# Optimization experiments

Hardware: AMD Instinct MI355X
Metric: run time of the kernel (lower is better)

## Reference

```python
import jax, jax.numpy as jnp
import numpy as np

B, C, H, W = 8, 256, 64, 64


def setup_inputs() -> dict:
    key = jax.random.key(0)
    ks = jax.random.split(key, 9)
    s = 1.0 / np.sqrt(C)  # conv2d default init scale
    return {
        "foreground": jax.random.normal(ks[0], (B, C, H, W), jnp.float32),
        "background": jax.random.normal(ks[1], (B, C, H, W), jnp.float32),
        "mask": jax.random.uniform(ks[2], (B, C, H, W), jnp.float32),
        "Wq": jax.random.normal(ks[3], (C, C), jnp.float32) * s,
        "bq": jnp.zeros((C,), jnp.float32),
        "Wk": jax.random.normal(ks[4], (C, C), jnp.float32) * s,
        "bk": jnp.zeros((C,), jnp.float32),
        "Wv": jax.random.normal(ks[5], (C, C), jnp.float32) * s,
        "bv": jnp.zeros((C,), jnp.float32),
        "gamma": jnp.ones((1,), jnp.float32),
    }


def _conv1x1(x, Wt, b):
    # 1x1 conv == per-pixel channel matmul; x: [B,C,H,W], Wt: [Cout,Cin]
    return jnp.einsum('bchw,oc->bohw', x, Wt) + b[None, :, None, None]


def reference(foreground, background, mask, Wq, bq, Wk, bk, Wv, bv, gamma):
    b, c, h, w = foreground.shape
    hw = h * w
    # mask is already at feature resolution (interpolate would be identity)
    q = _conv1x1(foreground, Wq, bq).reshape(b, c, hw)   # [B,C,HW]
    k = _conv1x1(background, Wk, bk).reshape(b, c, hw)   # [B,C,HW]
    # bmm(q, k^T): channel-channel correlation [B,C,C]
    corr = jnp.einsum('bci,bdi->bcd', q, k)
    m_r = mask.reshape(b, c, hw)                          # [B,C,HW]
    # bmm(corr, m_r): mask-modulated scores [B,C,HW]
    scores = jnp.einsum('bcd,bdi->bci', corr, m_r)
    energy = jax.nn.softmax(scores, axis=-1)
    v = _conv1x1(foreground, Wv, bv).reshape(b, c, hw)
    attended = (energy * v).reshape(b, c, h, w)
    out = foreground * mask + gamma[0] * (1.0 - mask) * attended
    return out
```

## Files before the change

### kernel.cpp

```cpp
#include <hip/hip_runtime.h>
#include <math.h>

#define B_    8
#define C_    256
#define HW_   4096
#define CHW_  ((long)C_ * HW_)

#define BKT   32
#define LDH   40
#define KS    16
#define KCH   (HW_ / KS)

typedef __attribute__((ext_vector_type(8))) short bf16x8;
typedef __attribute__((ext_vector_type(4))) float f32x4;
#define MFMA_BF16(a, b, c) __builtin_amdgcn_mfma_f32_16x16x32_bf16((a), (b), (c), 0, 0, 0)

__device__ __forceinline__ void cvt_hl4(const float4 f, uint* h, uint* l) {
    uint u0 = __float_as_uint(f.x), u1 = __float_as_uint(f.y),
         u2 = __float_as_uint(f.z), u3 = __float_as_uint(f.w);
    uint h0 = (u0 + 0x8000u) & 0xFFFF0000u, h1 = (u1 + 0x8000u) & 0xFFFF0000u,
         h2 = (u2 + 0x8000u) & 0xFFFF0000u, h3 = (u3 + 0x8000u) & 0xFFFF0000u;
    h[0] = (h0 >> 16) | h1;
    h[1] = (h2 >> 16) | h3;
    float l0 = f.x - __uint_as_float(h0), l1 = f.y - __uint_as_float(h1),
          l2 = f.z - __uint_as_float(h2), l3 = f.w - __uint_as_float(h3);
    uint a0 = __float_as_uint(l0) & 0xFFFF0000u, a1 = __float_as_uint(l1) & 0xFFFF0000u,
         a2 = __float_as_uint(l2) & 0xFFFF0000u, a3 = __float_as_uint(l3) & 0xFFFF0000u;
    l[0] = (a0 >> 16) | a1;
    l[1] = (a2 >> 16) | a3;
}
__device__ __forceinline__ void cvt_h4(const float4 f, uint* h) {
    uint u0 = __float_as_uint(f.x), u1 = __float_as_uint(f.y),
         u2 = __float_as_uint(f.z), u3 = __float_as_uint(f.w);
    uint h0 = (u0 + 0x8000u) & 0xFFFF0000u, h1 = (u1 + 0x8000u) & 0xFFFF0000u,
         h2 = (u2 + 0x8000u) & 0xFFFF0000u, h3 = (u3 + 0x8000u) & 0xFFFF0000u;
    h[0] = (h0 >> 16) | h1;
    h[1] = (h2 >> 16) | h3;
}

__global__ __launch_bounds__(256) void prep_hl(
    const float* __restrict__ fg, const float* __restrict__ bg,
    ushort* __restrict__ fgh, ushort* __restrict__ fgl,
    ushort* __restrict__ bgh, ushort* __restrict__ bgl,
    float* __restrict__ fsum, float* __restrict__ gsum)
{
    const int row = blockIdx.x;
    const int t   = threadIdx.x;
    const long base = (long)row * HW_;

    float sf = 0.0f, sg = 0.0f;
    #pragma unroll
    for (int j = 0; j < 4; ++j) {
        const int idx = (j * 256 + t) * 4;
        float4 a = *reinterpret_cast<const float4*>(&fg[base + idx]);
        float4 c = *reinterpret_cast<const float4*>(&bg[base + idx]);
        uint h[2], l[2];
        cvt_hl4(a, h, l);
        *reinterpret_cast<uint2*>(&fgh[base + idx]) = make_uint2(h[0], h[1]);
        *reinterpret_cast<uint2*>(&fgl[base + idx]) = make_uint2(l[0], l[1]);
        cvt_hl4(c, h, l);
        *reinterpret_cast<uint2*>(&bgh[base + idx]) = make_uint2(h[0], h[1]);
        *reinterpret_cast<uint2*>(&bgl[base + idx]) = make_uint2(l[0], l[1]);
        sf += a.x + a.y + a.z + a.w;
        sg += c.x + c.y + c.z + c.w;
    }
    #pragma unroll
    for (int o = 32; o > 0; o >>= 1) { sf += __shfl_xor(sf, o); sg += __shfl_xor(sg, o); }
    __shared__ float red[8];
    const int wid = t >> 6;
    if ((t & 63) == 0) { red[wid] = sf; red[4 + wid] = sg; }
    __syncthreads();
    if (t == 0) {
        fsum[row] = red[0] + red[1] + red[2] + red[3];
        gsum[row] = red[4] + red[5] + red[6] + red[7];
    }
}

__global__ __launch_bounds__(256) void conv_w(
    const float* __restrict__ Wv, ushort* __restrict__ Wvh)
{
    const int i = (blockIdx.x * 256 + threadIdx.x) * 4;
    float4 v = *reinterpret_cast<const float4*>(&Wv[i]);
    uint h[2];
    cvt_h4(v, h);
    *reinterpret_cast<uint2*>(&Wvh[i]) = make_uint2(h[0], h[1]);
}

__global__ __launch_bounds__(256) void conv_transpose(
    const float* __restrict__ mask, const float* __restrict__ fg,
    ushort* __restrict__ mTh, ushort* __restrict__ mTl, ushort* __restrict__ fTh)
{
    __shared__ float tile[64][65];
    const int zi = blockIdx.z;
    const bool domask = zi < B_;
    const int b = domask ? zi : zi - B_;
    const float* src = (domask ? mask : fg) + (long)b * CHW_;
    const int e0 = blockIdx.y * 64, i0 = blockIdx.x * 64;

    const int t  = threadIdx.x;
    const int tr = t >> 4, tc = (t & 15) * 4;

    #pragma unroll
    for (int j = 0; j < 4; ++j) {
        const int e = tr + j * 16;
        float4 v = *reinterpret_cast<const float4*>(&src[(long)(e0 + e) * HW_ + i0 + tc]);
        tile[e][tc + 0] = v.x; tile[e][tc + 1] = v.y;
        tile[e][tc + 2] = v.z; tile[e][tc + 3] = v.w;
    }
    __syncthreads();

    #pragma unroll
    for (int j = 0; j < 4; ++j) {
        const int i = tr + j * 16;
        float4 v = make_float4(tile[tc + 0][i], tile[tc + 1][i], tile[tc + 2][i], tile[tc + 3][i]);
        const long o = (long)b * CHW_ + (long)(i0 + i) * C_ + e0 + tc;
        if (domask) {
            uint h[2], l[2];
            cvt_hl4(v, h, l);
            *reinterpret_cast<uint2*>(&mTh[o]) = make_uint2(h[0], h[1]);
            *reinterpret_cast<uint2*>(&mTl[o]) = make_uint2(l[0], l[1]);
        } else {
            uint h[2];
            cvt_h4(v, h);
            *reinterpret_cast<uint2*>(&fTh[o]) = make_uint2(h[0], h[1]);
        }
    }
}

__global__ __launch_bounds__(256, 3) void gemm_nt_mfma(
    const ushort* __restrict__ Fh, const ushort* __restrict__ Fl,
    const ushort* __restrict__ Gh, const ushort* __restrict__ Gl,
    float* __restrict__ part)
{
    __shared__ ushort Ah[128 * LDH], Al[128 * LDH], Bh[128 * LDH], Bl[128 * LDH];

    const int z  = blockIdx.z;
    const int b  = z >> 4;
    const int ks = z & (KS - 1);
    const int c0 = blockIdx.y * 128;
    const int d0 = blockIdx.x * 128;
    const long boff = (long)b * CHW_ + (long)ks * KCH;

    const int t    = threadIdx.x;
    const int srow = t >> 1;
    const int sk   = (t & 1) * 16;
    const int lane = t & 63, w = t >> 6;
    const int col  = lane & 15, quad = lane >> 4;
    const int wm   = (w >> 1) * 64, wn = (w & 1) * 64;

    f32x4 acc[4][4] = {};

    for (int kt = 0; kt < KCH; kt += BKT) {
        const long ga = boff + (long)(c0 + srow) * HW_ + kt + sk;
        const long gb = boff + (long)(d0 + srow) * HW_ + kt + sk;
        uint4 ah0 = *reinterpret_cast<const uint4*>(&Fh[ga]);
        uint4 ah1 = *reinterpret_cast<const uint4*>(&Fh[ga + 8]);
        uint4 al0 = *reinterpret_cast<const uint4*>(&Fl[ga]);
        uint4 al1 = *reinterpret_cast<const uint4*>(&Fl[ga + 8]);
        uint4 bh0 = *reinterpret_cast<const uint4*>(&Gh[gb]);
        uint4 bh1 = *reinterpret_cast<const uint4*>(&Gh[gb + 8]);
        uint4 bl0 = *reinterpret_cast<const uint4*>(&Gl[gb]);
        uint4 bl1 = *reinterpret_cast<const uint4*>(&Gl[gb + 8]);
        *reinterpret_cast<uint4*>(&Ah[srow * LDH + sk])     = ah0;
        *reinterpret_cast<uint4*>(&Ah[srow * LDH + sk + 8]) = ah1;
        *reinterpret_cast<uint4*>(&Al[srow * LDH + sk])     = al0;
        *reinterpret_cast<uint4*>(&Al[srow * LDH + sk + 8]) = al1;
        *reinterpret_cast<uint4*>(&Bh[srow * LDH + sk])     = bh0;
        *reinterpret_cast<uint4*>(&Bh[srow * LDH + sk + 8]) = bh1;
        *reinterpret_cast<uint4*>(&Bl[srow * LDH + sk])     = bl0;
        *reinterpret_cast<uint4*>(&Bl[srow * LDH + sk + 8]) = bl1;
        __syncthreads();

        bf16x8 bfh[4], bfl[4];
        #pragma unroll
        for (int tj = 0; tj < 4; ++tj) {
            const int r = (wn + tj * 16 + col) * LDH + quad * 8;
            bfh[tj] = *reinterpret_cast<const bf16x8*>(&Bh[r]);
            bfl[tj] = *reinterpret_cast<const bf16x8*>(&Bl[r]);
        }
        #pragma unroll
        for (int ti = 0; ti < 4; ++ti) {
            const int r = (wm + ti * 16 + col) * LDH + quad * 8;
            bf16x8 afh = *reinterpret_cast<const bf16x8*>(&Ah[r]);
            bf16x8 afl = *reinterpret_cast<const bf16x8*>(&Al[r]);
            #pragma unroll
            for (int tj = 0; tj < 4; ++tj) {
                acc[ti][tj] = MFMA_BF16(afh, bfh[tj], acc[ti][tj]);
                acc[ti][tj] = MFMA_BF16(afh, bfl[tj], acc[ti][tj]);
                acc[ti][tj] = MFMA_BF16(afl, bfh[tj], acc[ti][tj]);
            }
        }
        __syncthreads();
    }

    float* P = part + (long)z * C_ * C_;
    #pragma unroll
    for (int ti = 0; ti < 4; ++ti) {
        const int m = c0 + wm + ti * 16 + quad * 4;
        #pragma unroll
        for (int tj = 0; tj < 4; ++tj) {
            const int n = d0 + wn + tj * 16 + col;
            #pragma unroll
            for (int r = 0; r < 4; ++r)
                P[(long)(m + r) * C_ + n] = acc[ti][tj][r];
        }
    }
}

__global__ __launch_bounds__(256, 3) void gemm_scores_mfma(
    const ushort* __restrict__ corrh, const ushort* __restrict__ corrl,
    const ushort* __restrict__ mTh,   const ushort* __restrict__ mTl,
    float* __restrict__ S)
{
    __shared__ ushort Ah[128 * LDH], Al[128 * LDH], Bh[128 * LDH], Bl[128 * LDH];

    const int b  = blockIdx.z;
    const int m0 = blockIdx.y * 128;
    const int n0 = blockIdx.x * 128;
    const ushort* Ahb = corrh + (long)b * C_ * C_;
    const ushort* Alb = corrl + (long)b * C_ * C_;
    const ushort* Bhb = mTh + (long)b * CHW_;
    const ushort* Blb = mTl + (long)b * CHW_;

    const int t    = threadIdx.x;
    const int srow = t >> 1;
    const int sk   = (t & 1) * 16;
    const int lane = t & 63, w = t >> 6;
    const int col  = lane & 15, quad = lane >> 4;
    const int wm   = (w >> 1) * 64, wn = (w & 1) * 64;

    f32x4 acc[4][4] = {};

    for (int kt = 0; kt < C_; kt += BKT) {
        const long ga = (long)(m0 + srow) * C_ + kt + sk;
        const long gb = (long)(n0 + srow) * C_ + kt + sk;
        uint4 ah0 = *reinterpret_cast<const uint4*>(&Ahb[ga]);
        uint4 ah1 = *reinterpret_cast<const uint4*>(&Ahb[ga + 8]);
        uint4 al0 = *reinterpret_cast<const uint4*>(&Alb[ga]);
        uint4 al1 = *reinterpret_cast<const uint4*>(&Alb[ga + 8]);
        uint4 bh0 = *reinterpret_cast<const uint4*>(&Bhb[gb]);
        uint4 bh1 = *reinterpret_cast<const uint4*>(&Bhb[gb + 8]);
        uint4 bl0 = *reinterpret_cast<const uint4*>(&Blb[gb]);
        uint4 bl1 = *reinterpret_cast<const uint4*>(&Blb[gb + 8]);
        *reinterpret_cast<uint4*>(&Ah[srow * LDH + sk])     = ah0;
        *reinterpret_cast<uint4*>(&Ah[srow * LDH + sk + 8]) = ah1;
        *reinterpret_cast<uint4*>(&Al[srow * LDH + sk])     = al0;
        *reinterpret_cast<uint4*>(&Al[srow * LDH + sk + 8]) = al1;
        *reinterpret_cast<uint4*>(&Bh[srow * LDH + sk])     = bh0;
        *reinterpret_cast<uint4*>(&Bh[srow * LDH + sk + 8]) = bh1;
        *reinterpret_cast<uint4*>(&Bl[srow * LDH + sk])     = bl0;
        *reinterpret_cast<uint4*>(&Bl[srow * LDH + sk + 8]) = bl1;
        __syncthreads();

        bf16x8 bfh[4], bfl[4];
        #pragma unroll
        for (int tj = 0; tj < 4; ++tj) {
            const int r = (wn + tj * 16 + col) * LDH + quad * 8;
            bfh[tj] = *reinterpret_cast<const bf16x8*>(&Bh[r]);
            bfl[tj] = *reinterpret_cast<const bf16x8*>(&Bl[r]);
        }
        #pragma unroll
        for (int ti = 0; ti < 4; ++ti) {
            const int r = (wm + ti * 16 + col) * LDH + quad * 8;
            bf16x8 afh = *reinterpret_cast<const bf16x8*>(&Ah[r]);
            bf16x8 afl = *reinterpret_cast<const bf16x8*>(&Al[r]);
            #pragma unroll
            for (int tj = 0; tj < 4; ++tj) {
                acc[ti][tj] = MFMA_BF16(afh, bfh[tj], acc[ti][tj]);
                acc[ti][tj] = MFMA_BF16(afh, bfl[tj], acc[ti][tj]);
                acc[ti][tj] = MFMA_BF16(afl, bfh[tj], acc[ti][tj]);
            }
        }
        __syncthreads();
    }

    float* Sb = S + (long)b * CHW_;
    #pragma unroll
    for (int ti = 0; ti < 4; ++ti) {
        const int m = m0 + wm + ti * 16 + quad * 4;
        #pragma unroll
        for (int tj = 0; tj < 4; ++tj) {
            const int n = n0 + wn + tj * 16 + col;
            #pragma unroll
            for (int r = 0; r < 4; ++r)
                Sb[(long)(m + r) * HW_ + n] = acc[ti][tj][r];
        }
    }
}

__global__ __launch_bounds__(256, 3) void gemm_v_final_mfma(
    const ushort* __restrict__ Wvh, const ushort* __restrict__ fTh,
    const float* __restrict__ bv, const float* __restrict__ fg,
    const float* __restrict__ mask, const float* __restrict__ S,
    const float* __restrict__ stats, const float* __restrict__ gamma,
    float* __restrict__ out)
{
    __shared__ ushort Ahh[128 * LDH], Bhh[128 * LDH];

    const int b  = blockIdx.z;
    const int m0 = blockIdx.y * 128;
    const int n0 = blockIdx.x * 128;
    const ushort* Bb = fTh + (long)b * CHW_;

    const int t    = threadIdx.x;
    const int srow = t >> 1;
    const int sk   = (t & 1) * 16;
    const int lane = t & 63, w = t >> 6;
    const int col  = lane & 15, quad = lane >> 4;
    const int wm   = (w >> 1) * 64, wn = (w & 1) * 64;

    f32x4 acc[4][4] = {};

    for (int kt = 0; kt < C_; kt += BKT) {
        const long ga = (long)(m0 + srow) * C_ + kt + sk;
        const long gb = (long)(n0 + srow) * C_ + kt + sk;
        uint4 a0 = *reinterpret_cast<const uint4*>(&Wvh[ga]);
        uint4 a1 = *reinterpret_cast<const uint4*>(&Wvh[ga + 8]);
        uint4 b0 = *reinterpret_cast<const uint4*>(&Bb[gb]);
        uint4 b1 = *reinterpret_cast<const uint4*>(&Bb[gb + 8]);
        *reinterpret_cast<uint4*>(&Ahh[srow * LDH + sk])     = a0;
        *reinterpret_cast<uint4*>(&Ahh[srow * LDH + sk + 8]) = a1;
        *reinterpret_cast<uint4*>(&Bhh[srow * LDH + sk])     = b0;
        *reinterpret_cast<uint4*>(&Bhh[srow * LDH + sk + 8]) = b1;
        __syncthreads();

        bf16x8 bfh[4];
        #pragma unroll
        for (int tj = 0; tj < 4; ++tj)
            bfh[tj] = *reinterpret_cast<const bf16x8*>(&Bhh[(wn + tj * 16 + col) * LDH + quad * 8]);
        #pragma unroll
        for (int ti = 0; ti < 4; ++ti) {
            bf16x8 afh = *reinterpret_cast<const bf16x8*>(&Ahh[(wm + ti * 16 + col) * LDH + quad * 8]);
            #pragma unroll
            for (int tj = 0; tj < 4; ++tj)
                acc[ti][tj] = MFMA_BF16(afh, bfh[tj], acc[ti][tj]);
        }
        __syncthreads();
    }

    const float g = gamma[0];
    #pragma unroll
    for (int ti = 0; ti < 4; ++ti) {
        const int m = m0 + wm + ti * 16 + quad * 4;
        #pragma unroll
        for (int r = 0; r < 4; ++r) {
            const int row  = b * C_ + m + r;
            const float mx  = stats[row];
            const float inv = 1.0f / stats[B_ * C_ + row];
            const float bvm = bv[m + r];
            #pragma unroll
            for (int tj = 0; tj < 4; ++tj) {
                const int n = n0 + wn + tj * 16 + col;
                const long e = (long)b * CHW_ + (long)(m + r) * HW_ + n;
                const float f  = fg[e];
                const float mk = mask[e];
                const float sv = S[e];
                const float vv = acc[ti][tj][r] + bvm;
                out[e] = f * mk + g * (1.0f - mk) * (__expf(sv - mx) * inv) * vv;
            }
        }
    }
}

__global__ __launch_bounds__(256) void reduce_part(
    const float* __restrict__ part, float* __restrict__ S1)
{
    const long idx = (long)blockIdx.x * 256 + threadIdx.x;
    const int  b   = (int)(idx >> 16);
    const long e   = idx & 65535;
    const float* p = part + ((long)b * KS) * 65536 + e;
    float s = 0.0f;
    #pragma unroll
    for (int ks = 0; ks < KS; ++ks) s += p[(long)ks * 65536];
    S1[idx] = s;
}

__global__ __launch_bounds__(256) void uvw_kernel(
    const float* __restrict__ Wq, const float* __restrict__ Wk,
    const float* __restrict__ bk,
    const float* __restrict__ fsum, const float* __restrict__ gsum,
    float* __restrict__ u, float* __restrict__ wh)
{
    const int g = blockIdx.x * 256 + threadIdx.x;
    if (g < 2048) {
        const int b = g >> 8, c = g & 255;
        const float* w = Wq + (long)c * C_;
        const float* s = fsum + b * C_;
        float acc = 0.0f;
        for (int e = 0; e < C_; ++e) acc = fmaf(w[e], s[e], acc);
        u[g] = acc;
    } else {
        const int g2 = g - 2048;
        const int b = g2 >> 8, d = g2 & 255;
        const float* w = Wk + (long)d * C_;
        const float* s = gsum + b * C_;
        float acc = 0.0f;
        for (int f = 0; f < C_; ++f) acc = fmaf(w[f], s[f], acc);
        wh[g2] = acc + (float)HW_ * bk[d];
    }
}

#define BK64 16
#define LDT64 68
__global__ __launch_bounds__(256) void gemm_nt64(
    const float* __restrict__ S1, const float* __restrict__ Wk,
    float* __restrict__ T)
{
    __shared__ float As[BK64][LDT64];
    __shared__ float Bs[BK64][LDT64];
    const int r0 = blockIdx.y * 64;
    const int d0 = blockIdx.x * 64;
    const int t   = threadIdx.x;
    const int tx  = t & 15, ty = t >> 4;
    const int tx4 = tx * 4, ty4 = ty * 4;
    const int am  = t >> 2, ak4 = (t & 3) * 4;

    float acc[4][4] = {};
    for (int k0 = 0; k0 < C_; k0 += BK64) {
        float4 av = *reinterpret_cast<const float4*>(&S1[(long)(r0 + am) * C_ + k0 + ak4]);
        float4 bw = *reinterpret_cast<const float4*>(&Wk[(long)(d0 + am) * C_ + k0 + ak4]);
        As[ak4+0][am]=av.x; As[ak4+1][am]=av.y; As[ak4+2][am]=av.z; As[ak4+3][am]=av.w;
        Bs[ak4+0][am]=bw.x; Bs[ak4+1][am]=bw.y; Bs[ak4+2][am]=bw.z; Bs[ak4+3][am]=bw.w;
        __syncthreads();
        #pragma unroll
        for (int kk = 0; kk < BK64; ++kk) {
            float4 a = *reinterpret_cast<const float4*>(&As[kk][ty4]);
            float4 x = *reinterpret_cast<const float4*>(&Bs[kk][tx4]);
            const float ar[4] = {a.x,a.y,a.z,a.w};
            const float xr[4] = {x.x,x.y,x.z,x.w};
            #pragma unroll
            for (int r = 0; r < 4; ++r)
                #pragma unroll
                for (int s = 0; s < 4; ++s)
                    acc[r][s] = fmaf(ar[r], xr[s], acc[r][s]);
        }
        __syncthreads();
    }
    #pragma unroll
    for (int r = 0; r < 4; ++r) {
        float4 o; o.x=acc[r][0]; o.y=acc[r][1]; o.z=acc[r][2]; o.w=acc[r][3];
        *reinterpret_cast<float4*>(&T[(long)(r0 + ty4 + r) * C_ + d0 + tx4]) = o;
    }
}

__global__ __launch_bounds__(256) void gemm_nn64_rank1(
    const float* __restrict__ Wq, const float* __restrict__ T,
    const float* __restrict__ u,  const float* __restrict__ bk,
    const float* __restrict__ bq, const float* __restrict__ wh,
    ushort* __restrict__ corrh, ushort* __restrict__ corrl)
{
    __shared__ float As[BK64][LDT64];
    __shared__ float Bs[BK64][LDT64];
    const int b  = blockIdx.z;
    const int m0 = blockIdx.y * 64;
    const int n0 = blockIdx.x * 64;
    const float* Tb = T + (long)b * C_ * C_;

    const int t   = threadIdx.x;
    const int tx  = t & 15, ty = t >> 4;
    const int tx4 = tx * 4, ty4 = ty * 4;
    const int am  = t >> 2, ak4 = (t & 3) * 4;
    const int xk  = ty,     xn4 = tx4;

    float acc[4][4] = {};
    for (int k0 = 0; k0 < C_; k0 += BK64) {
        float4 av = *reinterpret_cast<const float4*>(&Wq[(long)(m0 + am) * C_ + k0 + ak4]);
        float4 xv = *reinterpret_cast<const float4*>(&Tb[(long)(k0 + xk) * C_ + n0 + xn4]);
        As[ak4+0][am]=av.x; As[ak4+1][am]=av.y; As[ak4+2][am]=av.z; As[ak4+3][am]=av.w;
        *reinterpret_cast<float4*>(&Bs[xk][xn4]) = xv;
        __syncthreads();
        #pragma unroll
        for (int kk = 0; kk < BK64; ++kk) {
            float4 a = *reinterpret_cast<const float4*>(&As[kk][ty4]);
            float4 x = *reinterpret_cast<const float4*>(&Bs[kk][tx4]);
            const float ar[4] = {a.x,a.y,a.z,a.w};
            const float xr[4] = {x.x,x.y,x.z,x.w};
            #pragma unroll
            for (int r = 0; r < 4; ++r)
                #pragma unroll
                for (int s = 0; s < 4; ++s)
                    acc[r][s] = fmaf(ar[r], xr[s], acc[r][s]);
        }
        __syncthreads();
    }

    float4 bkv = *reinterpret_cast<const float4*>(&bk[n0 + tx4]);
    float4 whv = *reinterpret_cast<const float4*>(&wh[b * C_ + n0 + tx4]);
    #pragma unroll
    for (int r = 0; r < 4; ++r) {
        const int m = m0 + ty4 + r;
        const float um = u[b * C_ + m];
        const float bm = bq[m];
        float4 o;
        o.x = acc[r][0] + um*bkv.x + bm*whv.x;
        o.y = acc[r][1] + um*bkv.y + bm*whv.y;
        o.z = acc[r][2] + um*bkv.z + bm*whv.z;
        o.w = acc[r][3] + um*bkv.w + bm*whv.w;
        uint h[2], l[2];
        cvt_hl4(o, h, l);
        const long e = (long)b * C_ * C_ + (long)m * C_ + n0 + tx4;
        *reinterpret_cast<uint2*>(&corrh[e]) = make_uint2(h[0], h[1]);
        *reinterpret_cast<uint2*>(&corrl[e]) = make_uint2(l[0], l[1]);
    }
}

__global__ __launch_bounds__(256) void softmax_stats(
    const float* __restrict__ S, float* __restrict__ stats)
{
    const int row = blockIdx.x;
    const float* sr = S + (long)row * HW_;
    const int t = threadIdx.x;
    float4 x[4];
    #pragma unroll
    for (int j = 0; j < 4; ++j)
        x[j] = *reinterpret_cast<const float4*>(&sr[(j * 256 + t) * 4]);
    float m = -INFINITY;
    #pragma unroll
    for (int j = 0; j < 4; ++j)
        m = fmaxf(m, fmaxf(fmaxf(x[j].x, x[j].y), fmaxf(x[j].z, x[j].w)));
    __shared__ float red[8];
    #pragma unroll
    for (int o = 32; o > 0; o >>= 1) m = fmaxf(m, __shfl_xor(m, o));
    const int wid = t >> 6;
    if ((t & 63) == 0) red[wid] = m;
    __syncthreads();
    m = fmaxf(fmaxf(red[0], red[1]), fmaxf(red[2], red[3]));
    float sum = 0.0f;
    #pragma unroll
    for (int j = 0; j < 4; ++j)
        sum += __expf(x[j].x - m) + __expf(x[j].y - m)
             + __expf(x[j].z - m) + __expf(x[j].w - m);
    #pragma unroll
    for (int o = 32; o > 0; o >>= 1) sum += __shfl_xor(sum, o);
    if ((t & 63) == 0) red[4 + wid] = sum;
    __syncthreads();
    if (t == 0) {
        stats[row]            = m;
        stats[B_ * C_ + row]  = red[4] + red[5] + red[6] + red[7];
    }
}

extern "C" void kernel_launch(void* const* d_in, const int* in_sizes, int n_in,
                              void* d_out, int out_size, void* d_ws, size_t ws_size,
                              hipStream_t stream)
{
    const float* fg    = (const float*)d_in[0];
    const float* bg    = (const float*)d_in[1];
    const float* mask  = (const float*)d_in[2];
    const float* Wq    = (const float*)d_in[3];
    const float* bq    = (const float*)d_in[4];
    const float* Wk    = (const float*)d_in[5];
    const float* bk    = (const float*)d_in[6];
    const float* Wv    = (const float*)d_in[7];
    const float* bv    = (const float*)d_in[8];
    const float* gamma = (const float*)d_in[9];
    float* out = (float*)d_out;

    char* ws = (char*)d_ws;
    float*  part   = (float*)(ws);
    float*  scores = (float*)(ws);
    ushort* fgh    = (ushort*)(ws + 33554432);
    ushort* fgl    = (ushort*)(ws + 50331648);
    ushort* bgh    = (ushort*)(ws + 67108864);
    ushort* bgl    = (ushort*)(ws + 83886080);
    ushort* mTh    = (ushort*)(ws + 100663296);
    ushort* mTl    = (ushort*)(ws + 117440512);
    ushort* fTh    = (ushort*)(ws + 134217728);
    float*  S1     = (float*)(ws + 150994944);
    float*  T      = (float*)(ws + 153092096);
    ushort* corrh  = (ushort*)(ws + 155189248);
    ushort* corrl  = (ushort*)(ws + 156237824);
    ushort* Wvh    = (ushort*)(ws + 157286400);
    float*  stats  = (float*)(ws + 157417472);
    float*  fsum   = (float*)(ws + 157433856);
    float*  gsum   = (float*)(ws + 157442048);
    float*  u      = (float*)(ws + 157450240);
    float*  wh     = (float*)(ws + 157458432);

    const dim3 blk(256);

    prep_hl<<<dim3(B_ * C_), blk, 0, stream>>>(fg, bg, fgh, fgl, bgh, bgl, fsum, gsum);

    conv_transpose<<<dim3(HW_ / 64, C_ / 64, 2 * B_), blk, 0, stream>>>(
        mask, fg, mTh, mTl, fTh);
    conv_w<<<dim3(64), blk, 0, stream>>>(Wv, Wvh);

    gemm_nt_mfma<<<dim3(2, 2, B_ * KS), blk, 0, stream>>>(fgh, fgl, bgh, bgl, part);
    reduce_part<<<dim3(B_ * C_ * C_ / 256), blk, 0, stream>>>(part, S1);

    uvw_kernel<<<dim3(16), blk, 0, stream>>>(Wq, Wk, bk, fsum, gsum, u, wh);

    gemm_nt64<<<dim3(C_ / 64, B_ * C_ / 64), blk, 0, stream>>>(S1, Wk, T);
    gemm_nn64_rank1<<<dim3(4, 4, B_), blk, 0, stream>>>(Wq, T, u, bk, bq, wh, corrh, corrl);

    gemm_scores_mfma<<<dim3(HW_ / 128, C_ / 128, B_), blk, 0, stream>>>(
        corrh, corrl, mTh, mTl, scores);

    softmax_stats<<<dim3(B_ * C_), blk, 0, stream>>>(scores, stats);

    gemm_v_final_mfma<<<dim3(HW_ / 128, C_ / 128, B_), blk, 0, stream>>>(
        Wvh, fTh, bv, fg, mask, scores, stats, gamma, out);
}
```

Measured before the change: 317.3 us.

## Fuse bf16 split and row sums into GEMM; fuse softmax stats into scores GEMM

Drops the prep_hl kernel: the correlation GEMM now reads fp32 foreground/background directly, splits them into hi/lo bf16 in registers, and accumulates per-row sums through atomics into a zeroed buffer. Drops the separate softmax_stats pass: the scores GEMM computes per-tile row max and sum-exp in its epilogue, and a small combine kernel merges the 32 partials per row. The aim is to avoid writing and rereading 64MB of split bf16 data and a full extra read of the scores matrix. In exchange, the conversion work is repeated in every block that loads the same rows, and fp32 global loads are twice as large as the old bf16 loads.

```diff
diff --git a/kernel.cpp b/kernel.cpp
--- a/kernel.cpp
+++ b/kernel.cpp
@@ -38,44 +38,6 @@
     h[1] = (h2 >> 16) | h3;
 }
 
-__global__ __launch_bounds__(256) void prep_hl(
-    const float* __restrict__ fg, const float* __restrict__ bg,
-    ushort* __restrict__ fgh, ushort* __restrict__ fgl,
-    ushort* __restrict__ bgh, ushort* __restrict__ bgl,
-    float* __restrict__ fsum, float* __restrict__ gsum)
-{
-    const int row = blockIdx.x;
-    const int t   = threadIdx.x;
-    const long base = (long)row * HW_;
-
-    float sf = 0.0f, sg = 0.0f;
-    #pragma unroll
-    for (int j = 0; j < 4; ++j) {
-        const int idx = (j * 256 + t) * 4;
-        float4 a = *reinterpret_cast<const float4*>(&fg[base + idx]);
-        float4 c = *reinterpret_cast<const float4*>(&bg[base + idx]);
-        uint h[2], l[2];
-        cvt_hl4(a, h, l);
-        *reinterpret_cast<uint2*>(&fgh[base + idx]) = make_uint2(h[0], h[1]);
-        *reinterpret_cast<uint2*>(&fgl[base + idx]) = make_uint2(l[0], l[1]);
-        cvt_hl4(c, h, l);
-        *reinterpret_cast<uint2*>(&bgh[base + idx]) = make_uint2(h[0], h[1]);
-        *reinterpret_cast<uint2*>(&bgl[base + idx]) = make_uint2(l[0], l[1]);
-        sf += a.x + a.y + a.z + a.w;
-        sg += c.x + c.y + c.z + c.w;
-    }
-    #pragma unroll
-    for (int o = 32; o > 0; o >>= 1) { sf += __shfl_xor(sf, o); sg += __shfl_xor(sg, o); }
-    __shared__ float red[8];
-    const int wid = t >> 6;
-    if ((t & 63) == 0) { red[wid] = sf; red[4 + wid] = sg; }
-    __syncthreads();
-    if (t == 0) {
-        fsum[row] = red[0] + red[1] + red[2] + red[3];
-        gsum[row] = red[4] + red[5] + red[6] + red[7];
-    }
-}
-
 __global__ __launch_bounds__(256) void conv_w(
     const float* __restrict__ Wv, ushort* __restrict__ Wvh)
 {
@@ -128,9 +90,9 @@
 }
 
 __global__ __launch_bounds__(256, 3) void gemm_nt_mfma(
-    const ushort* __restrict__ Fh, const ushort* __restrict__ Fl,
-    const ushort* __restrict__ Gh, const ushort* __restrict__ Gl,
-    float* __restrict__ part)
+    const float* __restrict__ F, const float* __restrict__ G,
+    float* __restrict__ part,
+    float* __restrict__ fsum, float* __restrict__ gsum)
 {
     __shared__ ushort Ah[128 * LDH], Al[128 * LDH], Bh[128 * LDH], Bl[128 * LDH];
 
@@ -139,7 +101,10 @@
     const int ks = z & (KS - 1);
     const int c0 = blockIdx.y * 128;
     const int d0 = blockIdx.x * 128;
-    const long boff = (long)b * CHW_ + (long)ks * KCH;
+    const float* Fb = F + (long)b * CHW_ + (long)ks * KCH;
+    const float* Gb = G + (long)b * CHW_ + (long)ks * KCH;
+    const bool doF = (blockIdx.x == 0);
+    const bool doG = (blockIdx.y == 0);
 
     const int t    = threadIdx.x;
     const int srow = t >> 1;
@@ -149,26 +114,49 @@
     const int wm   = (w >> 1) * 64, wn = (w & 1) * 64;
 
     f32x4 acc[4][4] = {};
+    float rsF = 0.0f, rsG = 0.0f;
 
     for (int kt = 0; kt < KCH; kt += BKT) {
-        const long ga = boff + (long)(c0 + srow) * HW_ + kt + sk;
-        const long gb = boff + (long)(d0 + srow) * HW_ + kt + sk;
-        uint4 ah0 = *reinterpret_cast<const uint4*>(&Fh[ga]);
-        uint4 ah1 = *reinterpret_cast<const uint4*>(&Fh[ga + 8]);
-        uint4 al0 = *reinterpret_cast<const uint4*>(&Fl[ga]);
-        uint4 al1 = *reinterpret_cast<const uint4*>(&Fl[ga + 8]);
-        uint4 bh0 = *reinterpret_cast<const uint4*>(&Gh[gb]);
-        uint4 bh1 = *reinterpret_cast<const uint4*>(&Gh[gb + 8]);
-        uint4 bl0 = *reinterpret_cast<const uint4*>(&Gl[gb]);
-        uint4 bl1 = *reinterpret_cast<const uint4*>(&Gl[gb + 8]);
-        *reinterpret_cast<uint4*>(&Ah[srow * LDH + sk])     = ah0;
-        *reinterpret_cast<uint4*>(&Ah[srow * LDH + sk + 8]) = ah1;
-        *reinterpret_cast<uint4*>(&Al[srow * LDH + sk])     = al0;
-        *reinterpret_cast<uint4*>(&Al[srow * LDH + sk + 8]) = al1;
-        *reinterpret_cast<uint4*>(&Bh[srow * LDH + sk])     = bh0;
-        *reinterpret_cast<uint4*>(&Bh[srow * LDH + sk + 8]) = bh1;
-        *reinterpret_cast<uint4*>(&Bl[srow * LDH + sk])     = bl0;
-        *reinterpret_cast<uint4*>(&Bl[srow * LDH + sk + 8]) = bl1;
+        {
+            const float* s = &Fb[(long)(c0 + srow) * HW_ + kt + sk];
+            float4 v0 = *reinterpret_cast<const float4*>(s);
+            float4 v1 = *reinterpret_cast<const float4*>(s + 4);
+            float4 v2 = *reinterpret_cast<const float4*>(s + 8);
+            float4 v3 = *reinterpret_cast<const float4*>(s + 12);
+            if (doF) {
+                rsF += (v0.x + v0.y + v0.z + v0.w) + (v1.x + v1.y + v1.z + v1.w)
+                     + (v2.x + v2.y + v2.z + v2.w) + (v3.x + v3.y + v3.z + v3.w);
+            }
+            uint h[4], l[4];
+            cvt_hl4(v0, h + 0, l + 0);
+            cvt_hl4(v1, h + 2, l + 2);
+            *reinterpret_cast<uint4*>(&Ah[srow * LDH + sk]) = make_uint4(h[0], h[1], h[2], h[3]);
+            *reinterpret_cast<uint4*>(&Al[srow * LDH + sk]) = make_uint4(l[0], l[1], l[2], l[3]);
+            cvt_hl4(v2, h + 0, l + 0);
+            cvt_hl4(v3, h + 2, l + 2);
+            *reinterpret_cast<uint4*>(&Ah[srow * LDH + sk + 8]) = make_uint4(h[0], h[1], h[2], h[3]);
+            *reinterpret_cast<uint4*>(&Al[srow * LDH + sk + 8]) = make_uint4(l[0], l[1], l[2], l[3]);
+        }
+        {
+            const float* s = &Gb[(long)(d0 + srow) * HW_ + kt + sk];
+            float4 v0 = *reinterpret_cast<const float4*>(s);
+            float4 v1 = *reinterpret_cast<const float4*>(s + 4);
+            float4 v2 = *reinterpret_cast<const float4*>(s + 8);
+            float4 v3 = *reinterpret_cast<const float4*>(s + 12);
+            if (doG) {
+                rsG += (v0.x + v0.y + v0.z + v0.w) + (v1.x + v1.y + v1.z + v1.w)
+                     + (v2.x + v2.y + v2.z + v2.w) + (v3.x + v3.y + v3.z + v3.w);
+            }
+            uint h[4], l[4];
+            cvt_hl4(v0, h + 0, l + 0);
+            cvt_hl4(v1, h + 2, l + 2);
+            *reinterpret_cast<uint4*>(&Bh[srow * LDH + sk]) = make_uint4(h[0], h[1], h[2], h[3]);
+            *reinterpret_cast<uint4*>(&Bl[srow * LDH + sk]) = make_uint4(l[0], l[1], l[2], l[3]);
+            cvt_hl4(v2, h + 0, l + 0);
+            cvt_hl4(v3, h + 2, l + 2);
+            *reinterpret_cast<uint4*>(&Bh[srow * LDH + sk + 8]) = make_uint4(h[0], h[1], h[2], h[3]);
+            *reinterpret_cast<uint4*>(&Bl[srow * LDH + sk + 8]) = make_uint4(l[0], l[1], l[2], l[3]);
+        }
         __syncthreads();
 
         bf16x8 bfh[4], bfl[4];
@@ -193,6 +181,11 @@
         __syncthreads();
     }
 
+    rsF += __shfl_xor(rsF, 1);
+    rsG += __shfl_xor(rsG, 1);
+    if (doF && (t & 1) == 0) atomicAdd(&fsum[b * C_ + c0 + srow], rsF);
+    if (doG && (t & 1) == 0) atomicAdd(&gsum[b * C_ + d0 + srow], rsG);
+
     float* P = part + (long)z * C_ * C_;
     #pragma unroll
     for (int ti = 0; ti < 4; ++ti) {
@@ -210,9 +203,10 @@
 __global__ __launch_bounds__(256, 3) void gemm_scores_mfma(
     const ushort* __restrict__ corrh, const ushort* __restrict__ corrl,
     const ushort* __restrict__ mTh,   const ushort* __restrict__ mTl,
-    float* __restrict__ S)
+    float* __restrict__ S, float* __restrict__ pmax, float* __restrict__ psum)
 {
     __shared__ ushort Ah[128 * LDH], Al[128 * LDH], Bh[128 * LDH], Bl[128 * LDH];
+    __shared__ float pm[2][128], ps[2][128];
 
     const int b  = blockIdx.z;
     const int m0 = blockIdx.y * 128;
@@ -286,6 +280,56 @@
                 Sb[(long)(m + r) * HW_ + n] = acc[ti][tj][r];
         }
     }
+
+    #pragma unroll
+    for (int ti = 0; ti < 4; ++ti) {
+        #pragma unroll
+        for (int r = 0; r < 4; ++r) {
+            float mx = fmaxf(fmaxf(acc[ti][0][r], acc[ti][1][r]),
+                             fmaxf(acc[ti][2][r], acc[ti][3][r]));
+            mx = fmaxf(mx, __shfl_xor(mx, 1));
+            mx = fmaxf(mx, __shfl_xor(mx, 2));
+            mx = fmaxf(mx, __shfl_xor(mx, 4));
+            mx = fmaxf(mx, __shfl_xor(mx, 8));
+            float se = __expf(acc[ti][0][r] - mx) + __expf(acc[ti][1][r] - mx)
+                     + __expf(acc[ti][2][r] - mx) + __expf(acc[ti][3][r] - mx);
+            se += __shfl_xor(se, 1);
+            se += __shfl_xor(se, 2);
+            se += __shfl_xor(se, 4);
+            se += __shfl_xor(se, 8);
+            if (col == 0) {
+                const int rb = wm + ti * 16 + quad * 4 + r;
+                pm[w & 1][rb] = mx;
+                ps[w & 1][rb] = se;
+            }
+        }
+    }
+    __syncthreads();
+    if (t < 128) {
+        const float a0 = pm[0][t], a1 = pm[1][t];
+        const float gm = fmaxf(a0, a1);
+        const float gs = ps[0][t] * __expf(a0 - gm) + ps[1][t] * __expf(a1 - gm);
+        const long rowg = (long)b * C_ + m0 + t;
+        pmax[rowg * 32 + blockIdx.x] = gm;
+        psum[rowg * 32 + blockIdx.x] = gs;
+    }
+}
+
+__global__ __launch_bounds__(256) void combine_stats(
+    const float* __restrict__ pmax, const float* __restrict__ psum,
+    float* __restrict__ stats)
+{
+    const int row = blockIdx.x * 256 + threadIdx.x;
+    const float* pmr = pmax + (long)row * 32;
+    const float* psr = psum + (long)row * 32;
+    float gm = -INFINITY;
+    #pragma unroll
+    for (int i = 0; i < 32; ++i) gm = fmaxf(gm, pmr[i]);
+    float gs = 0.0f;
+    #pragma unroll
+    for (int i = 0; i < 32; ++i) gs += psr[i] * __expf(pmr[i] - gm);
+    stats[row]        = gm;
+    stats[2048 + row] = gs;
 }
 
 __global__ __launch_bounds__(256, 3) void gemm_v_final_mfma(
@@ -504,42 +548,6 @@
     }
 }
 
-__global__ __launch_bounds__(256) void softmax_stats(
-    const float* __restrict__ S, float* __restrict__ stats)
-{
-    const int row = blockIdx.x;
-    const float* sr = S + (long)row * HW_;
-    const int t = threadIdx.x;
-    float4 x[4];
-    #pragma unroll
-    for (int j = 0; j < 4; ++j)
-        x[j] = *reinterpret_cast<const float4*>(&sr[(j * 256 + t) * 4]);
-    float m = -INFINITY;
-    #pragma unroll
-    for (int j = 0; j < 4; ++j)
-        m = fmaxf(m, fmaxf(fmaxf(x[j].x, x[j].y), fmaxf(x[j].z, x[j].w)));
-    __shared__ float red[8];
-    #pragma unroll
-    for (int o = 32; o > 0; o >>= 1) m = fmaxf(m, __shfl_xor(m, o));
-    const int wid = t >> 6;
-    if ((t & 63) == 0) red[wid] = m;
-    __syncthreads();
-    m = fmaxf(fmaxf(red[0], red[1]), fmaxf(red[2], red[3]));
-    float sum = 0.0f;
-    #pragma unroll
-    for (int j = 0; j < 4; ++j)
-        sum += __expf(x[j].x - m) + __expf(x[j].y - m)
-             + __expf(x[j].z - m) + __expf(x[j].w - m);
-    #pragma unroll
-    for (int o = 32; o > 0; o >>= 1) sum += __shfl_xor(sum, o);
-    if ((t & 63) == 0) red[4 + wid] = sum;
-    __syncthreads();
-    if (t == 0) {
-        stats[row]            = m;
-        stats[B_ * C_ + row]  = red[4] + red[5] + red[6] + red[7];
-    }
-}
-
 extern "C" void kernel_launch(void* const* d_in, const int* in_sizes, int n_in,
                               void* d_out, int out_size, void* d_ws, size_t ws_size,
                               hipStream_t stream)
@@ -559,33 +567,31 @@
     char* ws = (char*)d_ws;
     float*  part   = (float*)(ws);
     float*  scores = (float*)(ws);
-    ushort* fgh    = (ushort*)(ws + 33554432);
-    ushort* fgl    = (ushort*)(ws + 50331648);
-    ushort* bgh    = (ushort*)(ws + 67108864);
-    ushort* bgl    = (ushort*)(ws + 83886080);
-    ushort* mTh    = (ushort*)(ws + 100663296);
-    ushort* mTl    = (ushort*)(ws + 117440512);
-    ushort* fTh    = (ushort*)(ws + 134217728);
-    float*  S1     = (float*)(ws + 150994944);
-    float*  T      = (float*)(ws + 153092096);
-    ushort* corrh  = (ushort*)(ws + 155189248);
-    ushort* corrl  = (ushort*)(ws + 156237824);
-    ushort* Wvh    = (ushort*)(ws + 157286400);
-    float*  stats  = (float*)(ws + 157417472);
-    float*  fsum   = (float*)(ws + 157433856);
-    float*  gsum   = (float*)(ws + 157442048);
-    float*  u      = (float*)(ws + 157450240);
-    float*  wh     = (float*)(ws + 157458432);
+    ushort* mTh    = (ushort*)(ws + 33554432);
+    ushort* mTl    = (ushort*)(ws + 50331648);
+    ushort* fTh    = (ushort*)(ws + 67108864);
+    float*  S1     = (float*)(ws + 83886080);
+    float*  T      = (float*)(ws + 85983232);
+    ushort* corrh  = (ushort*)(ws + 88080384);
+    ushort* corrl  = (ushort*)(ws + 89128960);
+    ushort* Wvh    = (ushort*)(ws + 90177536);
+    float*  stats  = (float*)(ws + 90308608);
+    float*  fsum   = (float*)(ws + 90324992);
+    float*  gsum   = (float*)(ws + 90333184);
+    float*  u      = (float*)(ws + 90341376);
+    float*  wh     = (float*)(ws + 90349568);
+    float*  pmax   = (float*)(ws + 90357760);
+    float*  psum   = (float*)(ws + 90619904);
 
     const dim3 blk(256);
 
-    prep_hl<<<dim3(B_ * C_), blk, 0, stream>>>(fg, bg, fgh, fgl, bgh, bgl, fsum, gsum);
+    hipMemsetAsync(fsum, 0, 16384, stream);
 
     conv_transpose<<<dim3(HW_ / 64, C_ / 64, 2 * B_), blk, 0, stream>>>(
         mask, fg, mTh, mTl, fTh);
     conv_w<<<dim3(64), blk, 0, stream>>>(Wv, Wvh);
 
-    gemm_nt_mfma<<<dim3(2, 2, B_ * KS), blk, 0, stream>>>(fgh, fgl, bgh, bgl, part);
+    gemm_nt_mfma<<<dim3(2, 2, B_ * KS), blk, 0, stream>>>(fg, bg, part, fsum, gsum);
     reduce_part<<<dim3(B_ * C_ * C_ / 256), blk, 0, stream>>>(part, S1);
 
     uvw_kernel<<<dim3(16), blk, 0, stream>>>(Wq, Wk, bk, fsum, gsum, u, wh);
@@ -594,9 +600,8 @@
     gemm_nn64_rank1<<<dim3(4, 4, B_), blk, 0, stream>>>(Wq, T, u, bk, bq, wh, corrh, corrl);
 
     gemm_scores_mfma<<<dim3(HW_ / 128, C_ / 128, B_), blk, 0, stream>>>(
-        corrh, corrl, mTh, mTl, scores);
-
-    softmax_stats<<<dim3(B_ * C_), blk, 0, stream>>>(scores, stats);
+        corrh, corrl, mTh, mTl, scores, pmax, psum);
+    combine_stats<<<dim3(8), blk, 0, stream>>>(pmax, psum, stats);
 
     gemm_v_final_mfma<<<dim3(HW_ / 128, C_ / 128, B_), blk, 0, stream>>>(
         Wvh, fTh, bv, fg, mask, scores, stats, gamma, out);
```

New measurement: 284.0 us. 10.5% less time.
